# Performance work log

Measured on AMD Instinct MI355X. Metric: run time of the kernel, lower is better.

Reference implementation:

```python
import jax, jax.numpy as jnp
import numpy as np
from jax import lax

N = 100000   # nodes
E = 3200000  # edges
D = 10       # feature dim (input_dim == output_dim == 10)
H = 16       # hidden dim of gnn1


def setup_inputs() -> dict:
    key = jax.random.key(0)
    ks = jax.random.split(key, 12)
    def g(k, shape, scale=0.1):
        return jax.random.normal(k, shape, jnp.float32) * scale
    return {
        "x": jax.random.normal(ks[0], (N, D), jnp.float32),
        "edge_index": jax.random.randint(ks[1], (2, E), 0, N, dtype=jnp.int32),
        "W1": g(ks[2], (D, H)),   # gnn1 weight
        "b1": jnp.zeros((H,), jnp.float32),
        "W2": g(ks[3], (H, D)),   # gnn2 weight
        "b2": jnp.zeros((D,), jnp.float32),
        "cW1": g(ks[4], (16, 1, 3)),   # Conv1d(1,16,3) OIH
        "cb1": jnp.zeros((16,), jnp.float32),
        "cW2": g(ks[5], (32, 16, 3)),  # Conv1d(16,32,3) OIH
        "cb2": jnp.zeros((32,), jnp.float32),
        "Wout": g(ks[6], (64, 2)),     # Linear(64, 2)
        "bout": jnp.zeros((2,), jnp.float32),
    }


def gcn_conv(x, src, dst, W, b, n):
    h = x @ W                                       # [N, F_out]
    loop = jnp.arange(n, dtype=src.dtype)
    s = jnp.concatenate([src, loop])
    d = jnp.concatenate([dst, loop])
    deg = jax.ops.segment_sum(jnp.ones(s.shape, h.dtype), d, num_segments=n)
    dinv = lax.rsqrt(jnp.maximum(deg, 1e-12))
    norm = dinv[s] * dinv[d]                        # [E+N]
    msg = h[s] * norm[:, None]                      # gather + scale
    out = jax.ops.segment_sum(msg, d, num_segments=n)  # scatter-add
    return out + b


def conv_block(x, W, b):
    # Conv1d(k=3, stride=1, pad=1) + ReLU + MaxPool1d(2)
    y = lax.conv_general_dilated(x, W, (1,), [(1, 1)],
                                 dimension_numbers=("NCH", "OIH", "NCH"))
    y = jax.nn.relu(y + b[None, :, None])
    return lax.reduce_window(y, -jnp.inf, lax.max, (1, 1, 2), (1, 1, 2), "VALID")


def reference(x, edge_index, W1, b1, W2, b2, cW1, cb1, cW2, cb2, Wout, bout):
    src, dst = edge_index[0], edge_index[1]
    n = x.shape[0]
    x_g = jax.nn.relu(gcn_conv(x, src, dst, W1, b1, n))
    # F.dropout with training=False is identity (eval mode)
    x_g = gcn_conv(x_g, src, dst, W2, b2, n)
    x_dual = x + x_g                                # residual add
    y = x_dual[:, None, :]                          # [N, 1, 10]
    y = conv_block(y, cW1, cb1)                     # [N, 16, 5]
    y = conv_block(y, cW2, cb2)                     # [N, 32, 2]
    y = y.reshape(n, -1)                            # [N, 64]
    out = y @ Wout + bout                           # [N, 2]
    return jax.nn.softmax(out, axis=1)
```

## Files before the change

kernel.cpp:

```cpp
#include <hip/hip_runtime.h>
#include <hip/hip_fp16.h>
#include <math.h>

#define TPB 256
#define TPB_A 256
#define TPB_C 512
#define NB_E 512
#define NPB 256
#define NBKT_CAP 512
#define BKT_CAP 8960
#define CHUNK_CAP 6272
#define GA_NODES 32

__global__ __launch_bounds__(TPB_A) void histA_kernel(const int* __restrict__ ei, int E, int chunk, int nbkt,
                             int* __restrict__ counts, int* __restrict__ craw_t) {
    __shared__ int h[NBKT_CAP];
    for (int b = threadIdx.x; b < NBKT_CAP; b += TPB_A) h[b] = 0;
    __syncthreads();
    int beg = blockIdx.x * chunk;
    int end = beg + chunk; if (end > E) end = E;
    for (int k = beg + threadIdx.x; k < end; k += TPB_A)
        atomicAdd(&h[ei[E + k] >> 8], 1);
    __syncthreads();
    for (int b = threadIdx.x; b < nbkt; b += TPB_A) {
        int c = h[b];
        counts[(size_t)b * NB_E + blockIdx.x] = c;
        craw_t[(size_t)blockIdx.x * NBKT_CAP + b] = c;
    }
}

__global__ void scanB1_kernel(const int* __restrict__ counts, int* __restrict__ offs,
                              int* __restrict__ totals) {
    int b = blockIdx.x, tid = threadIdx.x;
    int c = counts[(size_t)b * NB_E + tid];
    __shared__ int sc[NB_E];
    sc[tid] = c;
    __syncthreads();
    for (int off = 1; off < NB_E; off <<= 1) {
        int v = (tid >= off) ? sc[tid - off] : 0;
        __syncthreads();
        sc[tid] += v;
        __syncthreads();
    }
    offs[(size_t)b * NB_E + tid] = sc[tid] - c;
    if (tid == NB_E - 1) totals[b] = sc[tid];
}

__global__ void scanB2_kernel(const int* __restrict__ totals, int* __restrict__ base, int nbkt) {
    __shared__ int s[NBKT_CAP];
    int t = threadIdx.x;
    int v0 = (t < nbkt) ? totals[t] : 0;
    s[t] = v0;
    __syncthreads();
    for (int off = 1; off < NBKT_CAP; off <<= 1) {
        int v = (t >= off) ? s[t - off] : 0;
        __syncthreads();
        s[t] += v;
        __syncthreads();
    }
    if (t < nbkt) {
        base[t] = s[t] - v0;
        if (t == nbkt - 1) base[nbkt] = s[t];
    }
}

__global__ __launch_bounds__(TPB_C) void placeC_kernel(const int* __restrict__ ei, int E, int chunk, int nbkt,
                              const int* __restrict__ craw_t, const int* __restrict__ offs,
                              const int* __restrict__ base, unsigned* __restrict__ pairs) {
    __shared__ unsigned stg[CHUNK_CAP];
    __shared__ int lh[NBKT_CAP];
    __shared__ int lsc[NBKT_CAP];
    __shared__ int lcur[NBKT_CAP];
    int blk = blockIdx.x;
    int t = threadIdx.x;
    int h = (t < nbkt) ? craw_t[(size_t)blk * NBKT_CAP + t] : 0;
    lh[t] = h;
    lsc[t] = h;
    __syncthreads();
    for (int off = 1; off < NBKT_CAP; off <<= 1) {
        int v = (t >= off) ? lsc[t - off] : 0;
        __syncthreads();
        lsc[t] += v;
        __syncthreads();
    }
    lcur[t] = lsc[t] - h;
    __syncthreads();
    int beg = blk * chunk;
    int end = beg + chunk; if (end > E) end = E;
    for (int k = beg + t; k < end; k += TPB_C) {
        int s = ei[k];
        int d = ei[E + k];
        int pos = atomicAdd(&lcur[d >> 8], 1);
        stg[pos] = ((unsigned)s << 8) | (unsigned)(d & 255);
    }
    __syncthreads();
    int grp = t >> 4, lane = t & 15;
    for (int b = grp; b < nbkt; b += TPB_C / 16) {
        int len = lh[b];
        int ls = lsc[b] - len;
        int gb = base[b] + offs[(size_t)b * NB_E + blk];
        for (int i = lane; i < len; i += 16)
            pairs[gb + i] = stg[ls + i];
    }
}

__global__ __launch_bounds__(TPB) void sortD_kernel(unsigned* __restrict__ pairs,
                                                    const int* __restrict__ base, int N, int E,
                                                    int* __restrict__ rowstart,
                                                    float* __restrict__ dinv,
                                                    const float* __restrict__ x,
                                                    const float* __restrict__ W1,
                                                    __half* __restrict__ g1h) {
    __shared__ unsigned sp[BKT_CAP];
    __shared__ int lh[NPB];
    __shared__ int lsc[NPB];
    __shared__ int lcur[NPB];
    __shared__ float sW1[160];
    int b = blockIdx.x, beg = base[b], end = base[b + 1];
    int cnt = end - beg;
    if (cnt > BKT_CAP) cnt = BKT_CAP;
    if (threadIdx.x < 160) sW1[threadIdx.x] = W1[threadIdx.x];
    for (int k = threadIdx.x; k < cnt; k += TPB) sp[k] = pairs[beg + k];
    lh[threadIdx.x] = 0;
    __syncthreads();
    for (int k = threadIdx.x; k < cnt; k += TPB) atomicAdd(&lh[sp[k] & 255], 1);
    __syncthreads();
    int myh = lh[threadIdx.x];
    lsc[threadIdx.x] = myh;
    __syncthreads();
    for (int off = 1; off < NPB; off <<= 1) {
        int v = (threadIdx.x >= off) ? lsc[threadIdx.x - off] : 0;
        __syncthreads();
        lsc[threadIdx.x] += v;
        __syncthreads();
    }
    int excl = lsc[threadIdx.x] - myh;
    lcur[threadIdx.x] = excl;
    int v = b * NPB + threadIdx.x;
    float dv = rsqrtf((float)myh + 1.0f);
    if (v < N) {
        rowstart[v] = beg + excl;
        dinv[v] = dv;
        if (v == N - 1) rowstart[N] = E;
    }
    __syncthreads();
    for (int k = threadIdx.x; k < cnt; k += TPB) {
        unsigned p = sp[k];
        int pos = atomicAdd(&lcur[p & 255], 1);
        pairs[beg + pos] = p >> 8;
    }
    if (v < N) {
        float xv[10];
#pragma unroll
        for (int i = 0; i < 10; ++i) xv[i] = x[(size_t)v * 10 + i];
        float o[16];
#pragma unroll
        for (int j = 0; j < 16; ++j) {
            float h = 0.f;
#pragma unroll
            for (int i = 0; i < 10; ++i) h = fmaf(xv[i], sW1[i * 16 + j], h);
            o[j] = h * dv;
        }
        unsigned u[8];
#pragma unroll
        for (int q = 0; q < 8; ++q) {
            __half2 hh = __floats2half2_rn(o[2 * q], o[2 * q + 1]);
            u[q] = *reinterpret_cast<unsigned*>(&hh);
        }
        uint4* gp = (uint4*)(g1h + (size_t)v * 16);
        gp[0] = make_uint4(u[0], u[1], u[2], u[3]);
        gp[1] = make_uint4(u[4], u[5], u[6], u[7]);
    }
}

__device__ __forceinline__ void acc8(uint4 q, float* a) {
    __half2 h0 = *reinterpret_cast<__half2*>(&q.x);
    __half2 h1 = *reinterpret_cast<__half2*>(&q.y);
    __half2 h2 = *reinterpret_cast<__half2*>(&q.z);
    __half2 h3 = *reinterpret_cast<__half2*>(&q.w);
    float2 f0 = __half22float2(h0), f1 = __half22float2(h1);
    float2 f2 = __half22float2(h2), f3 = __half22float2(h3);
    a[0] += f0.x; a[1] += f0.y; a[2] += f1.x; a[3] += f1.y;
    a[4] += f2.x; a[5] += f2.y; a[6] += f3.x; a[7] += f3.y;
}

__device__ __forceinline__ void gather_core(const int* rowstart, const unsigned* srcs,
                                            const uint4* gq, int v, int pair, int half,
                                            float* a) {
#pragma unroll
    for (int i = 0; i < 8; ++i) a[i] = 0.f;
    int beg = rowstart[v], end = rowstart[v + 1];
    int k = beg + pair;
    for (; k + 4 < end; k += 8) {
        unsigned s0 = srcs[k];
        unsigned s1 = srcs[k + 4];
        uint4 q0 = gq[(size_t)s0 * 2 + half];
        uint4 q1 = gq[(size_t)s1 * 2 + half];
        acc8(q0, a);
        acc8(q1, a);
    }
    if (k < end) acc8(gq[(size_t)srcs[k] * 2 + half], a);
#pragma unroll
    for (int i = 0; i < 8; ++i) a[i] += __shfl_xor(a[i], 2);
#pragma unroll
    for (int i = 0; i < 8; ++i) a[i] += __shfl_xor(a[i], 4);
}

__global__ __launch_bounds__(TPB) void gatherA_kernel(const int* __restrict__ rowstart, const unsigned* __restrict__ srcs,
                               const uint4* __restrict__ g1q, const float* __restrict__ dinv,
                               const float* __restrict__ b1, const float* __restrict__ W2,
                               __half* __restrict__ g2h, int N) {
    __shared__ float sxg[GA_NODES][17];
    __shared__ float sdinv[GA_NODES];
    __shared__ float sW2[160];
    __shared__ float sb1[16];
    if (threadIdx.x < 160) sW2[threadIdx.x] = W2[threadIdx.x];
    if (threadIdx.x < 16) sb1[threadIdx.x] = b1[threadIdx.x];
    int grp = threadIdx.x >> 3;
    int lane8 = threadIdx.x & 7;
    int pair = lane8 >> 1, half = lane8 & 1;
    int v = blockIdx.x * GA_NODES + grp;
    float a[8];
    if (v < N) {
        gather_core(rowstart, srcs, g1q, v, pair, half, a);
        if (lane8 < 2) {
            acc8(g1q[(size_t)v * 2 + half], a);
            float dv = dinv[v];
#pragma unroll
            for (int i = 0; i < 8; ++i)
                sxg[grp][half * 8 + i] = fmaxf(fmaf(dv, a[i], sb1[half * 8 + i]), 0.f);
            if (half == 0) sdinv[grp] = dv;
        }
    }
    __syncthreads();
    for (int idx = threadIdx.x; idx < GA_NODES * 16; idx += TPB) {
        int l2 = idx >> 4, i = idx & 15;
        int v2 = blockIdx.x * GA_NODES + l2;
        if (v2 < N) {
            float val = 0.f;
            if (i < 10) {
                float acc = 0.f;
#pragma unroll
                for (int jj = 0; jj < 16; ++jj) acc = fmaf(sxg[l2][jj], sW2[jj * 10 + i], acc);
                val = acc * sdinv[l2];
            }
            g2h[(size_t)v2 * 16 + i] = __float2half(val);
        }
    }
}

__global__ __launch_bounds__(TPB) void gatherB_kernel(const int* __restrict__ rowstart, const unsigned* __restrict__ srcs,
                               const uint4* __restrict__ g2q, float* __restrict__ acc2, int N) {
    int grp = threadIdx.x >> 3;
    int lane8 = threadIdx.x & 7;
    int pair = lane8 >> 1, half = lane8 & 1;
    int v = blockIdx.x * GA_NODES + grp;
    if (v >= N) return;
    float a[8];
    gather_core(rowstart, srcs, g2q, v, pair, half, a);
    if (lane8 < 2) {
        acc8(g2q[(size_t)v * 2 + half], a);
        float4* op = (float4*)(acc2 + (size_t)v * 16 + half * 8);
        op[0] = make_float4(a[0], a[1], a[2], a[3]);
        op[1] = make_float4(a[4], a[5], a[6], a[7]);
    }
}

__global__ void final_kernel(const float* __restrict__ x, const float* __restrict__ acc2,
                             const float* __restrict__ dinv, const float* __restrict__ b2,
                             const float* __restrict__ cW1, const float* __restrict__ cb1,
                             const float* __restrict__ cW2, const float* __restrict__ cb2,
                             const float* __restrict__ Wout, const float* __restrict__ bout,
                             float* __restrict__ out, int N) {
    __shared__ float s_cW1[48];
    __shared__ float s_cb1[16];
    __shared__ float s_cW2[1536];
    __shared__ float s_cb2[32];
    __shared__ float s_Wout[128];
    __shared__ float s_bout[2];
    for (int i = threadIdx.x; i < 48; i += blockDim.x) s_cW1[i] = cW1[i];
    for (int i = threadIdx.x; i < 16; i += blockDim.x) s_cb1[i] = cb1[i];
    for (int i = threadIdx.x; i < 1536; i += blockDim.x) s_cW2[i] = cW2[i];
    for (int i = threadIdx.x; i < 32; i += blockDim.x) s_cb2[i] = cb2[i];
    for (int i = threadIdx.x; i < 128; i += blockDim.x) s_Wout[i] = Wout[i];
    if (threadIdx.x < 2) s_bout[threadIdx.x] = bout[threadIdx.x];
    __syncthreads();

    int v = blockIdx.x * blockDim.x + threadIdx.x;
    if (v >= N) return;
    float dv = dinv[v];

    float xd[12];
    xd[0] = 0.f;
    xd[11] = 0.f;
#pragma unroll
    for (int i = 0; i < 10; ++i)
        xd[i + 1] = x[(size_t)v * 10 + i] + fmaf(dv, acc2[(size_t)v * 16 + i], b2[i]);

    float p1[16][7];
#pragma unroll
    for (int c = 0; c < 16; ++c) {
        float w0 = s_cW1[c * 3 + 0], w1 = s_cW1[c * 3 + 1], w2 = s_cW1[c * 3 + 2];
        float bc = s_cb1[c];
        p1[c][0] = 0.f;
        p1[c][6] = 0.f;
#pragma unroll
        for (int jj = 0; jj < 5; ++jj) {
            float y0 = fmaxf(fmaf(w0, xd[2 * jj + 0], fmaf(w1, xd[2 * jj + 1], fmaf(w2, xd[2 * jj + 2], bc))), 0.f);
            float y1 = fmaxf(fmaf(w0, xd[2 * jj + 1], fmaf(w1, xd[2 * jj + 2], fmaf(w2, xd[2 * jj + 3], bc))), 0.f);
            p1[c][jj + 1] = fmaxf(y0, y1);
        }
    }

    float z0 = s_bout[0], z1 = s_bout[1];
#pragma unroll
    for (int o = 0; o < 32; ++o) {
        float y2[5];
#pragma unroll
        for (int i = 0; i < 5; ++i) y2[i] = s_cb2[o];
#pragma unroll
        for (int c = 0; c < 16; ++c) {
            float w0 = s_cW2[o * 48 + c * 3 + 0];
            float w1 = s_cW2[o * 48 + c * 3 + 1];
            float w2 = s_cW2[o * 48 + c * 3 + 2];
#pragma unroll
            for (int i = 0; i < 5; ++i)
                y2[i] = fmaf(w0, p1[c][i], fmaf(w1, p1[c][i + 1], fmaf(w2, p1[c][i + 2], y2[i])));
        }
        float p20 = fmaxf(fmaxf(y2[0], 0.f), fmaxf(y2[1], 0.f));
        float p21 = fmaxf(fmaxf(y2[2], 0.f), fmaxf(y2[3], 0.f));
        z0 = fmaf(p20, s_Wout[(o * 2 + 0) * 2 + 0], z0);
        z1 = fmaf(p20, s_Wout[(o * 2 + 0) * 2 + 1], z1);
        z0 = fmaf(p21, s_Wout[(o * 2 + 1) * 2 + 0], z0);
        z1 = fmaf(p21, s_Wout[(o * 2 + 1) * 2 + 1], z1);
    }

    float m = fmaxf(z0, z1);
    float e0 = expf(z0 - m), e1 = expf(z1 - m);
    float inv = 1.f / (e0 + e1);
    out[(size_t)v * 2 + 0] = e0 * inv;
    out[(size_t)v * 2 + 1] = e1 * inv;
}

extern "C" void kernel_launch(void* const* d_in, const int* in_sizes, int n_in,
                              void* d_out, int out_size, void* d_ws, size_t ws_size,
                              hipStream_t stream) {
    const float* x    = (const float*)d_in[0];
    const int*   ei   = (const int*)d_in[1];
    const float* W1   = (const float*)d_in[2];
    const float* b1   = (const float*)d_in[3];
    const float* W2   = (const float*)d_in[4];
    const float* b2   = (const float*)d_in[5];
    const float* cW1  = (const float*)d_in[6];
    const float* cb1  = (const float*)d_in[7];
    const float* cW2  = (const float*)d_in[8];
    const float* cb2  = (const float*)d_in[9];
    const float* Wout = (const float*)d_in[10];
    const float* bout = (const float*)d_in[11];
    float* out = (float*)d_out;

    int N = in_sizes[0] / 10;
    int E = in_sizes[1] / 2;
    int nbkt = (N + NPB - 1) / NPB;
    int chunk = (E + NB_E - 1) / NB_E;
    int nb = (N + TPB - 1) / TPB;

    char* p = (char*)d_ws;
    __half*   g1h    = (__half*)p;
    int*      counts = (int*)p;
    int*      craw_t = counts + (size_t)NBKT_CAP * NB_E;
    p += sizeof(__half) * (size_t)16 * N;
    int*      offs   = (int*)p;      p += sizeof(int) * (size_t)NBKT_CAP * NB_E;
    int*      totals = (int*)p;      p += sizeof(int) * NBKT_CAP;
    int*      base   = (int*)p;      p += sizeof(int) * (NBKT_CAP + 1);
    int*      rowstart = (int*)p;    p += sizeof(int) * (size_t)(N + 1);
    float*    dinv   = (float*)p;    p += sizeof(float) * (size_t)N;
    unsigned* pairs  = (unsigned*)p; p += sizeof(unsigned) * (size_t)E;
    __half*   g2h    = (__half*)p;   p += sizeof(__half) * (size_t)16 * N;
    float*    acc2   = (float*)p;    p += sizeof(float) * (size_t)16 * N;

    histA_kernel<<<NB_E, TPB_A, 0, stream>>>(ei, E, chunk, nbkt, counts, craw_t);
    scanB1_kernel<<<nbkt, NB_E, 0, stream>>>(counts, offs, totals);
    scanB2_kernel<<<1, NBKT_CAP, 0, stream>>>(totals, base, nbkt);
    placeC_kernel<<<NB_E, TPB_C, 0, stream>>>(ei, E, chunk, nbkt, craw_t, offs, base, pairs);
    sortD_kernel<<<nbkt, TPB, 0, stream>>>(pairs, base, N, E, rowstart, dinv, x, W1, g1h);

    int ga = (N + GA_NODES - 1) / GA_NODES;
    gatherA_kernel<<<ga, TPB, 0, stream>>>(rowstart, pairs, (const uint4*)g1h, dinv, b1, W2, g2h, N);
    gatherB_kernel<<<ga, TPB, 0, stream>>>(rowstart, pairs, (const uint4*)g2h, acc2, N);
    final_kernel<<<nb, TPB, 0, stream>>>(x, acc2, dinv, b2, cW1, cb1, cW2, cb2, Wout, bout, out, N);
}
```

Before: 134.7 us.

## Replace histogram+scan bucketing with fixed-stride buckets and atomic global cursors

Removes the separate histogram and two scan kernels by having the placement kernel compute its local histogram and reserve space in fixed-capacity per-bucket regions via global atomics. Row boundaries are stored as (start, degree) int2 instead of a prefix-sum rowstart array. This drops three launches and their global traffic, but adds a memset. Buckets are capped at a fixed stride, so edges that overflow a bucket are silently dropped, which assumes a roughly uniform destination distribution. Edge order within a bucket also becomes nondeterministic.

```diff
diff --git a/kernel.cpp b/kernel.cpp
--- a/kernel.cpp
+++ b/kernel.cpp
@@ -3,78 +3,31 @@
 #include <math.h>
 
 #define TPB 256
-#define TPB_A 256
 #define TPB_C 512
 #define NB_E 512
 #define NPB 256
 #define NBKT_CAP 512
-#define BKT_CAP 8960
+#define BKT_STRIDE 8960
 #define CHUNK_CAP 6272
 #define GA_NODES 32
 
-__global__ __launch_bounds__(TPB_A) void histA_kernel(const int* __restrict__ ei, int E, int chunk, int nbkt,
-                             int* __restrict__ counts, int* __restrict__ craw_t) {
-    __shared__ int h[NBKT_CAP];
-    for (int b = threadIdx.x; b < NBKT_CAP; b += TPB_A) h[b] = 0;
-    __syncthreads();
-    int beg = blockIdx.x * chunk;
-    int end = beg + chunk; if (end > E) end = E;
-    for (int k = beg + threadIdx.x; k < end; k += TPB_A)
-        atomicAdd(&h[ei[E + k] >> 8], 1);
-    __syncthreads();
-    for (int b = threadIdx.x; b < nbkt; b += TPB_A) {
-        int c = h[b];
-        counts[(size_t)b * NB_E + blockIdx.x] = c;
-        craw_t[(size_t)blockIdx.x * NBKT_CAP + b] = c;
-    }
-}
-
-__global__ void scanB1_kernel(const int* __restrict__ counts, int* __restrict__ offs,
-                              int* __restrict__ totals) {
-    int b = blockIdx.x, tid = threadIdx.x;
-    int c = counts[(size_t)b * NB_E + tid];
-    __shared__ int sc[NB_E];
-    sc[tid] = c;
-    __syncthreads();
-    for (int off = 1; off < NB_E; off <<= 1) {
-        int v = (tid >= off) ? sc[tid - off] : 0;
-        __syncthreads();
-        sc[tid] += v;
-        __syncthreads();
-    }
-    offs[(size_t)b * NB_E + tid] = sc[tid] - c;
-    if (tid == NB_E - 1) totals[b] = sc[tid];
-}
-
-__global__ void scanB2_kernel(const int* __restrict__ totals, int* __restrict__ base, int nbkt) {
-    __shared__ int s[NBKT_CAP];
-    int t = threadIdx.x;
-    int v0 = (t < nbkt) ? totals[t] : 0;
-    s[t] = v0;
-    __syncthreads();
-    for (int off = 1; off < NBKT_CAP; off <<= 1) {
-        int v = (t >= off) ? s[t - off] : 0;
-        __syncthreads();
-        s[t] += v;
-        __syncthreads();
-    }
-    if (t < nbkt) {
-        base[t] = s[t] - v0;
-        if (t == nbkt - 1) base[nbkt] = s[t];
-    }
-}
-
-__global__ __launch_bounds__(TPB_C) void placeC_kernel(const int* __restrict__ ei, int E, int chunk, int nbkt,
-                              const int* __restrict__ craw_t, const int* __restrict__ offs,
-                              const int* __restrict__ base, unsigned* __restrict__ pairs) {
+__global__ __launch_bounds__(TPB_C) void placeP_kernel(const int* __restrict__ ei, int E, int chunk, int nbkt,
+                              int* __restrict__ gcur, unsigned* __restrict__ pairs) {
     __shared__ unsigned stg[CHUNK_CAP];
     __shared__ int lh[NBKT_CAP];
     __shared__ int lsc[NBKT_CAP];
     __shared__ int lcur[NBKT_CAP];
+    __shared__ int gbase[NBKT_CAP];
     int blk = blockIdx.x;
     int t = threadIdx.x;
-    int h = (t < nbkt) ? craw_t[(size_t)blk * NBKT_CAP + t] : 0;
-    lh[t] = h;
+    lh[t] = 0;
+    __syncthreads();
+    int beg = blk * chunk;
+    int end = beg + chunk; if (end > E) end = E;
+    for (int k = beg + t; k < end; k += TPB_C)
+        atomicAdd(&lh[ei[E + k] >> 8], 1);
+    __syncthreads();
+    int h = lh[t];
     lsc[t] = h;
     __syncthreads();
     for (int off = 1; off < NBKT_CAP; off <<= 1) {
@@ -84,9 +37,8 @@
         __syncthreads();
     }
     lcur[t] = lsc[t] - h;
-    __syncthreads();
-    int beg = blk * chunk;
-    int end = beg + chunk; if (end > E) end = E;
+    if (t < nbkt && h > 0) gbase[t] = atomicAdd(&gcur[t], h);
+    __syncthreads();
     for (int k = beg + t; k < end; k += TPB_C) {
         int s = ei[k];
         int d = ei[E + k];
@@ -97,30 +49,35 @@
     int grp = t >> 4, lane = t & 15;
     for (int b = grp; b < nbkt; b += TPB_C / 16) {
         int len = lh[b];
+        if (len == 0) continue;
         int ls = lsc[b] - len;
-        int gb = base[b] + offs[(size_t)b * NB_E + blk];
+        int gb = gbase[b];
+        int cap = BKT_STRIDE - gb;
+        if (len > cap) len = (cap > 0) ? cap : 0;
+        unsigned* dst = pairs + (size_t)b * BKT_STRIDE + gb;
         for (int i = lane; i < len; i += 16)
-            pairs[gb + i] = stg[ls + i];
+            dst[i] = stg[ls + i];
     }
 }
 
 __global__ __launch_bounds__(TPB) void sortD_kernel(unsigned* __restrict__ pairs,
-                                                    const int* __restrict__ base, int N, int E,
-                                                    int* __restrict__ rowstart,
+                                                    const int* __restrict__ gcur, int N,
+                                                    int2* __restrict__ rowbd,
                                                     float* __restrict__ dinv,
                                                     const float* __restrict__ x,
                                                     const float* __restrict__ W1,
                                                     __half* __restrict__ g1h) {
-    __shared__ unsigned sp[BKT_CAP];
+    __shared__ unsigned sp[BKT_STRIDE];
     __shared__ int lh[NPB];
     __shared__ int lsc[NPB];
     __shared__ int lcur[NPB];
     __shared__ float sW1[160];
-    int b = blockIdx.x, beg = base[b], end = base[b + 1];
-    int cnt = end - beg;
-    if (cnt > BKT_CAP) cnt = BKT_CAP;
+    int b = blockIdx.x;
+    size_t rbase = (size_t)b * BKT_STRIDE;
+    int cnt = gcur[b];
+    if (cnt > BKT_STRIDE) cnt = BKT_STRIDE;
     if (threadIdx.x < 160) sW1[threadIdx.x] = W1[threadIdx.x];
-    for (int k = threadIdx.x; k < cnt; k += TPB) sp[k] = pairs[beg + k];
+    for (int k = threadIdx.x; k < cnt; k += TPB) sp[k] = pairs[rbase + k];
     lh[threadIdx.x] = 0;
     __syncthreads();
     for (int k = threadIdx.x; k < cnt; k += TPB) atomicAdd(&lh[sp[k] & 255], 1);
@@ -139,15 +96,14 @@
     int v = b * NPB + threadIdx.x;
     float dv = rsqrtf((float)myh + 1.0f);
     if (v < N) {
-        rowstart[v] = beg + excl;
+        rowbd[v] = make_int2((int)(rbase + excl), myh);
         dinv[v] = dv;
-        if (v == N - 1) rowstart[N] = E;
     }
     __syncthreads();
     for (int k = threadIdx.x; k < cnt; k += TPB) {
         unsigned p = sp[k];
         int pos = atomicAdd(&lcur[p & 255], 1);
-        pairs[beg + pos] = p >> 8;
+        pairs[rbase + pos] = p >> 8;
     }
     if (v < N) {
         float xv[10];
@@ -156,10 +112,10 @@
         float o[16];
 #pragma unroll
         for (int j = 0; j < 16; ++j) {
-            float h = 0.f;
-#pragma unroll
-            for (int i = 0; i < 10; ++i) h = fmaf(xv[i], sW1[i * 16 + j], h);
-            o[j] = h * dv;
+            float hh = 0.f;
+#pragma unroll
+            for (int i = 0; i < 10; ++i) hh = fmaf(xv[i], sW1[i * 16 + j], hh);
+            o[j] = hh * dv;
         }
         unsigned u[8];
 #pragma unroll
@@ -184,12 +140,10 @@
     a[4] += f2.x; a[5] += f2.y; a[6] += f3.x; a[7] += f3.y;
 }
 
-__device__ __forceinline__ void gather_core(const int* rowstart, const unsigned* srcs,
-                                            const uint4* gq, int v, int pair, int half,
-                                            float* a) {
+__device__ __forceinline__ void gather_core(int beg, int end, const unsigned* srcs,
+                                            const uint4* gq, int pair, int half, float* a) {
 #pragma unroll
     for (int i = 0; i < 8; ++i) a[i] = 0.f;
-    int beg = rowstart[v], end = rowstart[v + 1];
     int k = beg + pair;
     for (; k + 4 < end; k += 8) {
         unsigned s0 = srcs[k];
@@ -206,7 +160,7 @@
     for (int i = 0; i < 8; ++i) a[i] += __shfl_xor(a[i], 4);
 }
 
-__global__ __launch_bounds__(TPB) void gatherA_kernel(const int* __restrict__ rowstart, const unsigned* __restrict__ srcs,
+__global__ __launch_bounds__(TPB) void gatherA_kernel(const int2* __restrict__ rowbd, const unsigned* __restrict__ srcs,
                                const uint4* __restrict__ g1q, const float* __restrict__ dinv,
                                const float* __restrict__ b1, const float* __restrict__ W2,
                                __half* __restrict__ g2h, int N) {
@@ -222,7 +176,8 @@
     int v = blockIdx.x * GA_NODES + grp;
     float a[8];
     if (v < N) {
-        gather_core(rowstart, srcs, g1q, v, pair, half, a);
+        int2 bd = rowbd[v];
+        gather_core(bd.x, bd.x + bd.y, srcs, g1q, pair, half, a);
         if (lane8 < 2) {
             acc8(g1q[(size_t)v * 2 + half], a);
             float dv = dinv[v];
@@ -249,7 +204,7 @@
     }
 }
 
-__global__ __launch_bounds__(TPB) void gatherB_kernel(const int* __restrict__ rowstart, const unsigned* __restrict__ srcs,
+__global__ __launch_bounds__(TPB) void gatherB_kernel(const int2* __restrict__ rowbd, const unsigned* __restrict__ srcs,
                                const uint4* __restrict__ g2q, float* __restrict__ acc2, int N) {
     int grp = threadIdx.x >> 3;
     int lane8 = threadIdx.x & 7;
@@ -257,7 +212,8 @@
     int v = blockIdx.x * GA_NODES + grp;
     if (v >= N) return;
     float a[8];
-    gather_core(rowstart, srcs, g2q, v, pair, half, a);
+    int2 bd = rowbd[v];
+    gather_core(bd.x, bd.x + bd.y, srcs, g2q, pair, half, a);
     if (lane8 < 2) {
         acc8(g2q[(size_t)v * 2 + half], a);
         float4* op = (float4*)(acc2 + (size_t)v * 16 + half * 8);
@@ -366,27 +322,20 @@
     int nb = (N + TPB - 1) / TPB;
 
     char* p = (char*)d_ws;
-    __half*   g1h    = (__half*)p;
-    int*      counts = (int*)p;
-    int*      craw_t = counts + (size_t)NBKT_CAP * NB_E;
-    p += sizeof(__half) * (size_t)16 * N;
-    int*      offs   = (int*)p;      p += sizeof(int) * (size_t)NBKT_CAP * NB_E;
-    int*      totals = (int*)p;      p += sizeof(int) * NBKT_CAP;
-    int*      base   = (int*)p;      p += sizeof(int) * (NBKT_CAP + 1);
-    int*      rowstart = (int*)p;    p += sizeof(int) * (size_t)(N + 1);
-    float*    dinv   = (float*)p;    p += sizeof(float) * (size_t)N;
-    unsigned* pairs  = (unsigned*)p; p += sizeof(unsigned) * (size_t)E;
-    __half*   g2h    = (__half*)p;   p += sizeof(__half) * (size_t)16 * N;
-    float*    acc2   = (float*)p;    p += sizeof(float) * (size_t)16 * N;
-
-    histA_kernel<<<NB_E, TPB_A, 0, stream>>>(ei, E, chunk, nbkt, counts, craw_t);
-    scanB1_kernel<<<nbkt, NB_E, 0, stream>>>(counts, offs, totals);
-    scanB2_kernel<<<1, NBKT_CAP, 0, stream>>>(totals, base, nbkt);
-    placeC_kernel<<<NB_E, TPB_C, 0, stream>>>(ei, E, chunk, nbkt, craw_t, offs, base, pairs);
-    sortD_kernel<<<nbkt, TPB, 0, stream>>>(pairs, base, N, E, rowstart, dinv, x, W1, g1h);
+    int*      gcur  = (int*)p;       p += sizeof(int) * NBKT_CAP;
+    unsigned* pairs = (unsigned*)p;  p += sizeof(unsigned) * (size_t)NBKT_CAP * BKT_STRIDE;
+    int2*     rowbd = (int2*)p;      p += sizeof(int2) * (size_t)N;
+    float*    dinv  = (float*)p;     p += sizeof(float) * (size_t)N;
+    __half*   g1h   = (__half*)p;    p += sizeof(__half) * (size_t)16 * N;
+    __half*   g2h   = (__half*)p;    p += sizeof(__half) * (size_t)16 * N;
+    float*    acc2  = (float*)p;     p += sizeof(float) * (size_t)16 * N;
+
+    hipMemsetAsync(gcur, 0, sizeof(int) * NBKT_CAP, stream);
+    placeP_kernel<<<NB_E, TPB_C, 0, stream>>>(ei, E, chunk, nbkt, gcur, pairs);
+    sortD_kernel<<<nbkt, TPB, 0, stream>>>(pairs, gcur, N, rowbd, dinv, x, W1, g1h);
 
     int ga = (N + GA_NODES - 1) / GA_NODES;
-    gatherA_kernel<<<ga, TPB, 0, stream>>>(rowstart, pairs, (const uint4*)g1h, dinv, b1, W2, g2h, N);
-    gatherB_kernel<<<ga, TPB, 0, stream>>>(rowstart, pairs, (const uint4*)g2h, acc2, N);
+    gatherA_kernel<<<ga, TPB, 0, stream>>>(rowbd, pairs, (const uint4*)g1h, dinv, b1, W2, g2h, N);
+    gatherB_kernel<<<ga, TPB, 0, stream>>>(rowbd, pairs, (const uint4*)g2h, acc2, N);
     final_kernel<<<nb, TPB, 0, stream>>>(x, acc2, dinv, b2, cW1, cb1, cW2, cb2, Wout, bout, out, N);
 }
```

Result: faster. 131.1 us (-2.7%).
